# Kernel tuning notes

Measured on AMD Instinct MI355X. Metric: run time of the kernel, lower is better.

Reference implementation:

```python
import jax, jax.numpy as jnp
import numpy as np

# Dimensions
N = 20000      # nodes
E = 320000     # edges (avg degree 16)
B = 4          # batchsize (independent weight replicas)
F_IN = 128     # nfeat
H = 128        # nhid[0]
C = 64         # nclass


def setup_inputs() -> dict:
    key = jax.random.key(0)
    ks = jax.random.split(key, 9)
    x = jax.random.normal(ks[0], (N, F_IN), dtype=jnp.float32)
    adj_rows = jax.random.randint(ks[1], (E,), 0, N, dtype=jnp.int32)
    adj_cols = jax.random.randint(ks[2], (E,), 0, N, dtype=jnp.int32)
    # positive normalized-ish edge weights (like a normalized adjacency)
    adj_vals = jax.random.uniform(ks[3], (E,), dtype=jnp.float32) / 16.0
    # GraphConvolution weights: uniform(-stdv, stdv), stdv = 1/sqrt(out_features)
    s0 = 1.0 / np.sqrt(H)
    s1 = 1.0 / np.sqrt(C)
    w0 = jax.random.uniform(ks[4], (B, F_IN, H), dtype=jnp.float32, minval=-s0, maxval=s0)
    w1 = jax.random.uniform(ks[5], (B, H, C), dtype=jnp.float32, minval=-s1, maxval=s1)
    # per-batch Linear(nclass, 1) heads, stacked
    sr = 1.0 / np.sqrt(C)
    reg_w = jax.random.uniform(ks[6], (B, C), dtype=jnp.float32, minval=-sr, maxval=sr)
    reg_b = jax.random.uniform(ks[7], (B,), dtype=jnp.float32, minval=-sr, maxval=sr)
    return dict(x=x, adj_rows=adj_rows, adj_cols=adj_cols, adj_vals=adj_vals,
                w0=w0, w1=w1, reg_w=reg_w, reg_b=reg_b)


def _gcn_layer(h, w, rows, cols, vals):
    # h: [N, B, in], w: [B, in, out]
    support = jnp.einsum('nbi,bio->nbo', h, w)          # per-batch dense GEMM
    s_flat = support.reshape(N, -1)                     # [N, B*out]
    # spmm: out[r] += val * s_flat[c] for each edge (r, c)
    msgs = vals[:, None] * s_flat[cols]                 # [E, B*out]
    out = jax.ops.segment_sum(msgs, rows, num_segments=N)
    return out.reshape(N, B, -1)                        # [N, B, out]


def reference(x, adj_rows, adj_cols, adj_vals, w0, w1, reg_w, reg_b):
    # eval mode: dropout is identity
    h = jnp.broadcast_to(x[:, None, :], (N, B, F_IN))   # expand + transpose(0,1)
    h = jax.nn.relu(_gcn_layer(h, w0, adj_rows, adj_cols, adj_vals))
    h = _gcn_layer(h, w1, adj_rows, adj_cols, adj_vals)  # [N, B, C]
    hT = h.transpose(1, 0, 2)                            # [B, N, C]
    y = jnp.einsum('bnc,bc->bn', hT, reg_w) + reg_b[:, None]
    return y
```

## Files before the change

### kernel.cpp

```cpp
#include <hip/hip_runtime.h>
#include <hip/hip_bf16.h>


#define NN 20000
#define EE 320000
#define BB 4
#define FF 128
#define HH 128
#define CC 64
#define DEGW 64

typedef unsigned short u16;
typedef short short8 __attribute__((ext_vector_type(8)));
typedef float floatx4 __attribute__((ext_vector_type(4)));

static __device__ __forceinline__ float b2f(u16 u) {
    union { unsigned int i; float f; } x;
    x.i = ((unsigned int)u) << 16;
    return x.f;
}

static __device__ __forceinline__ u16 f2b(float f) {
    __hip_bfloat16 h = __float2bfloat16(f);
    return *reinterpret_cast<u16*>(&h);
}


__global__ void k_pre(int* __restrict__ deg,
                      const float* __restrict__ x, u16* __restrict__ xb,
                      const float* __restrict__ w0, const float* __restrict__ w1,
                      const float* __restrict__ regw, u16* __restrict__ w0t,
                      float* __restrict__ v1) {
    int gid = blockIdx.x * 256 + threadIdx.x;
    if (gid < NN) deg[gid] = 0;
    if (gid < NN * FF / 4) {
        float4 v = ((const float4*)x)[gid];
        ushort4 o;
        o.x = f2b(v.x); o.y = f2b(v.y); o.z = f2b(v.z); o.w = f2b(v.w);
        ((ushort4*)xb)[gid] = o;
    }
    if (gid < BB * FF * HH) {
        int b = gid >> 14;
        int rem = gid & 16383;
        int h = rem >> 7;
        int k = rem & 127;
        w0t[gid] = f2b(w0[(b << 14) + (k << 7) + h]);
    }
    if (gid < BB * HH) {
        int b = gid >> 7;
        int h = gid & 127;
        const float* wrow = w1 + (b * HH + h) * CC;
        const float* rw = regw + b * CC;
        float s = 0.f;
#pragma unroll
        for (int c = 0; c < CC; ++c) s += wrow[c] * rw[c];
        v1[gid] = s;
    }
}


__global__ void k_scatter(const int* __restrict__ rows, const int* __restrict__ cols,
                          const float* __restrict__ vals, int* __restrict__ deg,
                          uint2* __restrict__ epack) {
    int e = blockIdx.x * 256 + threadIdx.x;
    if (e < EE) {
        int r = rows[e];
        int p = atomicAdd(&deg[r], 1);
        epack[(r << 6) + p] = make_uint2((unsigned)cols[e], __float_as_uint(vals[e]));
    }
}


__global__ void k_spmm(const int* __restrict__ deg, const uint2* __restrict__ epack,
                       const u16* __restrict__ xb, u16* __restrict__ xa) {
    int wave = (blockIdx.x * 256 + threadIdx.x) >> 6;
    int lane = threadIdx.x & 63;
    if (wave >= NN) return;
    int d = deg[wave];
    int eg = lane >> 3;
    int fl = lane & 7;
    int p0 = wave << 6;
    float acc[16];
#pragma unroll
    for (int j = 0; j < 16; ++j) acc[j] = 0.f;
    for (int p = eg; p < d; p += 8) {
        uint2 ep = epack[p0 + p];
        float v = __uint_as_float(ep.y);
        const u16* xr = xb + (((size_t)ep.x) << 7) + fl * 16;
        short8 x0 = *(const short8*)(xr);
        short8 x1 = *(const short8*)(xr + 8);
#pragma unroll
        for (int j = 0; j < 8; ++j) {
            acc[j]     += v * b2f((u16)x0[j]);
            acc[8 + j] += v * b2f((u16)x1[j]);
        }
    }
#pragma unroll
    for (int j = 0; j < 16; ++j) {
        acc[j] += __shfl_xor(acc[j], 8);
        acc[j] += __shfl_xor(acc[j], 16);
        acc[j] += __shfl_xor(acc[j], 32);
    }
    if (eg == 0) {
        short8 o0, o1;
#pragma unroll
        for (int j = 0; j < 8; ++j) {
            o0[j] = (short)f2b(acc[j]);
            o1[j] = (short)f2b(acc[8 + j]);
        }
        u16* orow = xa + (((size_t)wave) << 7) + fl * 16;
        *(short8*)(orow) = o0;
        *(short8*)(orow + 8) = o1;
    }
}


__global__ __launch_bounds__(256) void k_gemm(const u16* __restrict__ xa,
                                              const u16* __restrict__ w0t,
                                              const float* __restrict__ v1,
                                              float* __restrict__ z) {
    __shared__ u16 sA[128 * 64];
    __shared__ u16 sB[128 * 64];
    __shared__ float part[2][128];

    int b = blockIdx.y;
    int rowbase = blockIdx.x * 128;
    int t = threadIdx.x;
    int wid = t >> 6;
    int lane = t & 63;
    int wr = wid >> 1;
    int wc = wid & 1;
    int g = lane >> 4;
    int lr = lane & 15;

    floatx4 acc[4][4];
#pragma unroll
    for (int i = 0; i < 4; ++i)
#pragma unroll
        for (int j = 0; j < 4; ++j) acc[i][j] = (floatx4){0.f, 0.f, 0.f, 0.f};

#pragma unroll
    for (int ks = 0; ks < 2; ++ks) {
#pragma unroll
        for (int it = 0; it < 4; ++it) {
            int idx = it * 256 + t;
            int r = idx >> 3;
            int c = idx & 7;
            int sl = c ^ (r & 7);
            uint4 av = make_uint4(0u, 0u, 0u, 0u);
            int grow = rowbase + r;
            if (grow < NN) av = *(const uint4*)(xa + (((size_t)grow) << 7) + ks * 64 + c * 8);
            *(uint4*)(&sA[r * 64 + sl * 8]) = av;
            uint4 bv = *(const uint4*)(w0t + (((size_t)b) << 14) + (r << 7) + ks * 64 + c * 8);
            *(uint4*)(&sB[r * 64 + sl * 8]) = bv;
        }
        __syncthreads();

#pragma unroll
        for (int kk = 0; kk < 2; ++kk) {
            short8 a[4], bv[4];
#pragma unroll
            for (int i = 0; i < 4; ++i) {
                int row = wr * 64 + i * 16 + lr;
                int slot = (kk * 4 + g) ^ (row & 7);
                a[i] = *(const short8*)(&sA[row * 64 + slot * 8]);
            }
#pragma unroll
            for (int j = 0; j < 4; ++j) {
                int h = wc * 64 + j * 16 + lr;
                int slot = (kk * 4 + g) ^ (h & 7);
                bv[j] = *(const short8*)(&sB[h * 64 + slot * 8]);
            }
#pragma unroll
            for (int i = 0; i < 4; ++i)
#pragma unroll
                for (int j = 0; j < 4; ++j)
                    acc[i][j] = __builtin_amdgcn_mfma_f32_16x16x32_bf16(a[i], bv[j], acc[i][j], 0, 0, 0);
        }
        __syncthreads();
    }

    float vv[4];
#pragma unroll
    for (int j = 0; j < 4; ++j) vv[j] = v1[b * 128 + wc * 64 + j * 16 + lr];

#pragma unroll
    for (int i = 0; i < 4; ++i) {
#pragma unroll
        for (int r = 0; r < 4; ++r) {
            float s = 0.f;
#pragma unroll
            for (int j = 0; j < 4; ++j) s += fmaxf(acc[i][j][r], 0.f) * vv[j];
            s += __shfl_xor(s, 1);
            s += __shfl_xor(s, 2);
            s += __shfl_xor(s, 4);
            s += __shfl_xor(s, 8);
            if (lr == 0) part[wc][wr * 64 + i * 16 + g * 4 + r] = s;
        }
    }
    __syncthreads();
    if (t < 128) {
        int grow = rowbase + t;
        if (grow < NN) z[grow * 4 + b] = part[0][t] + part[1][t];
    }
}


__global__ void k_spmv(const int* __restrict__ deg, const uint2* __restrict__ epack,
                       const float* __restrict__ z, const float* __restrict__ regb,
                       float* __restrict__ y) {
    int wave = (blockIdx.x * 256 + threadIdx.x) >> 6;
    int lane = threadIdx.x & 63;
    if (wave >= NN) return;
    int d = deg[wave];
    int eg = lane >> 2;
    int b = lane & 3;
    int p0 = wave << 6;
    float acc = 0.f;
    for (int p = eg; p < d; p += 16) {
        uint2 ep = epack[p0 + p];
        acc += __uint_as_float(ep.y) * z[(((size_t)ep.x) << 2) + b];
    }
    acc += __shfl_xor(acc, 4);
    acc += __shfl_xor(acc, 8);
    acc += __shfl_xor(acc, 16);
    acc += __shfl_xor(acc, 32);
    if (lane < 4) y[lane * NN + wave] = acc + regb[lane];
}


extern "C" void kernel_launch(void* const* d_in, const int* in_sizes, int n_in,
                              void* d_out, int out_size, void* d_ws, size_t ws_size,
                              hipStream_t stream) {
    const float* x    = (const float*)d_in[0];
    const int*   rows = (const int*)d_in[1];
    const int*   cols = (const int*)d_in[2];
    const float* vals = (const float*)d_in[3];
    const float* w0   = (const float*)d_in[4];
    const float* w1   = (const float*)d_in[5];
    const float* regw = (const float*)d_in[6];
    const float* regb = (const float*)d_in[7];
    float* y = (float*)d_out;

    char* ws = (char*)d_ws;
    int*   deg   = (int*)(ws + 0);
    uint2* epack = (uint2*)(ws + 81920);
    u16*   xb    = (u16*)(ws + 10321920);
    u16*   xa    = (u16*)(ws + 15441920);
    u16*   w0t   = (u16*)(ws + 20561920);
    float* v1    = (float*)(ws + 20692992);
    float* z     = (float*)(ws + 20695040);

    k_pre<<<(NN * FF / 4 + 255) / 256, 256, 0, stream>>>(deg, x, xb, w0, w1, regw, w0t, v1);
    k_scatter<<<(EE + 255) / 256, 256, 0, stream>>>(rows, cols, vals, deg, epack);
    k_spmm<<<(NN * 64) / 256, 256, 0, stream>>>(deg, epack, xb, xa);
    dim3 ggemm((NN + 127) / 128, BB);
    k_gemm<<<ggemm, 256, 0, stream>>>(xa, w0t, v1, z);
    k_spmv<<<(NN * 64 + 255) / 256, 256, 0, stream>>>(deg, epack, z, regb, y);
}
```

Baseline: 127.4 us.

## Fuse SpMM with per-batch GEMM and merge scatter into preprocessing kernel

The SpMM is fused with the first-layer GEMM. Each 512-thread block aggregates 64 rows into swizzled shared memory, then runs the MFMA GEMM for all four batch replicas on those rows, so the intermediate xa never travels through global memory. The edge scatter moves into the init kernel, and the degree counters are zeroed with a memset instead, which removes one kernel launch. In exchange, the B operand is now read directly from global memory rather than staged in LDS, and the fused block runs the latency-bound gather and the MFMA phases one after the other with no overlap.

Result: slower. 155.0 us (+21.6%).

```diff
diff --git a/kernel.cpp b/kernel.cpp
--- a/kernel.cpp
+++ b/kernel.cpp
@@ -8,7 +8,6 @@
 #define FF 128
 #define HH 128
 #define CC 64
-#define DEGW 64
 
 typedef unsigned short u16;
 typedef short short8 __attribute__((ext_vector_type(8)));
@@ -26,13 +25,19 @@
 }
 
 
-__global__ void k_pre(int* __restrict__ deg,
-                      const float* __restrict__ x, u16* __restrict__ xb,
-                      const float* __restrict__ w0, const float* __restrict__ w1,
-                      const float* __restrict__ regw, u16* __restrict__ w0t,
-                      float* __restrict__ v1) {
+__global__ void k_init(const int* __restrict__ rows, const int* __restrict__ cols,
+                       const float* __restrict__ vals, int* __restrict__ deg,
+                       uint2* __restrict__ epack,
+                       const float* __restrict__ x, u16* __restrict__ xb,
+                       const float* __restrict__ w0, const float* __restrict__ w1,
+                       const float* __restrict__ regw, u16* __restrict__ w0t,
+                       float* __restrict__ v1) {
     int gid = blockIdx.x * 256 + threadIdx.x;
-    if (gid < NN) deg[gid] = 0;
+    if (gid < EE) {
+        int r = rows[gid];
+        int p = atomicAdd(&deg[r], 1);
+        epack[(r << 6) + p] = make_uint2((unsigned)cols[gid], __float_as_uint(vals[gid]));
+    }
     if (gid < NN * FF / 4) {
         float4 v = ((const float4*)x)[gid];
         ushort4 o;
@@ -59,149 +64,124 @@
 }
 
 
-__global__ void k_scatter(const int* __restrict__ rows, const int* __restrict__ cols,
-                          const float* __restrict__ vals, int* __restrict__ deg,
-                          uint2* __restrict__ epack) {
-    int e = blockIdx.x * 256 + threadIdx.x;
-    if (e < EE) {
-        int r = rows[e];
-        int p = atomicAdd(&deg[r], 1);
-        epack[(r << 6) + p] = make_uint2((unsigned)cols[e], __float_as_uint(vals[e]));
-    }
-}
-
-
-__global__ void k_spmm(const int* __restrict__ deg, const uint2* __restrict__ epack,
-                       const u16* __restrict__ xb, u16* __restrict__ xa) {
-    int wave = (blockIdx.x * 256 + threadIdx.x) >> 6;
-    int lane = threadIdx.x & 63;
-    if (wave >= NN) return;
-    int d = deg[wave];
-    int eg = lane >> 3;
-    int fl = lane & 7;
-    int p0 = wave << 6;
-    float acc[16];
-#pragma unroll
-    for (int j = 0; j < 16; ++j) acc[j] = 0.f;
-    for (int p = eg; p < d; p += 8) {
-        uint2 ep = epack[p0 + p];
-        float v = __uint_as_float(ep.y);
-        const u16* xr = xb + (((size_t)ep.x) << 7) + fl * 16;
-        short8 x0 = *(const short8*)(xr);
-        short8 x1 = *(const short8*)(xr + 8);
-#pragma unroll
-        for (int j = 0; j < 8; ++j) {
-            acc[j]     += v * b2f((u16)x0[j]);
-            acc[8 + j] += v * b2f((u16)x1[j]);
+__global__ __launch_bounds__(512) void k_spmm_gemm(const int* __restrict__ deg,
+                                                   const uint2* __restrict__ epack,
+                                                   const u16* __restrict__ xb,
+                                                   const u16* __restrict__ w0t,
+                                                   const float* __restrict__ v1,
+                                                   float* __restrict__ z) {
+    __shared__ u16 sA[64 * 128];
+    __shared__ float part[BB][2][64];
+
+    int base = blockIdx.x * 64;
+    int t = threadIdx.x;
+    int wv = t >> 6;
+    int lane = t & 63;
+
+    {
+        int eg = lane >> 3;
+        int fl = lane & 7;
+#pragma unroll
+        for (int it = 0; it < 8; ++it) {
+            int lr0 = wv * 8 + it;
+            int row = base + lr0;
+            int d = (row < NN) ? deg[row] : 0;
+            float acc[16];
+#pragma unroll
+            for (int j = 0; j < 16; ++j) acc[j] = 0.f;
+            int p0 = row << 6;
+            for (int p = eg; p < d; p += 8) {
+                uint2 ep = epack[p0 + p];
+                float v = __uint_as_float(ep.y);
+                const u16* xr = xb + (((size_t)ep.x) << 7) + fl * 16;
+                short8 x0 = *(const short8*)(xr);
+                short8 x1 = *(const short8*)(xr + 8);
+#pragma unroll
+                for (int j = 0; j < 8; ++j) {
+                    acc[j]     += v * b2f((u16)x0[j]);
+                    acc[8 + j] += v * b2f((u16)x1[j]);
+                }
+            }
+#pragma unroll
+            for (int j = 0; j < 16; ++j) {
+                acc[j] += __shfl_xor(acc[j], 8);
+                acc[j] += __shfl_xor(acc[j], 16);
+                acc[j] += __shfl_xor(acc[j], 32);
+            }
+            if (eg == 0) {
+                short8 o0, o1;
+#pragma unroll
+                for (int j = 0; j < 8; ++j) {
+                    o0[j] = (short)f2b(acc[j]);
+                    o1[j] = (short)f2b(acc[8 + j]);
+                }
+                int c0 = 2 * fl, c1 = 2 * fl + 1;
+                *(short8*)(&sA[lr0 * 128 + (c0 ^ (lr0 & 7)) * 8]) = o0;
+                *(short8*)(&sA[lr0 * 128 + (c1 ^ (lr0 & 7)) * 8]) = o1;
+            }
         }
     }
-#pragma unroll
-    for (int j = 0; j < 16; ++j) {
-        acc[j] += __shfl_xor(acc[j], 8);
-        acc[j] += __shfl_xor(acc[j], 16);
-        acc[j] += __shfl_xor(acc[j], 32);
-    }
-    if (eg == 0) {
-        short8 o0, o1;
-#pragma unroll
-        for (int j = 0; j < 8; ++j) {
-            o0[j] = (short)f2b(acc[j]);
-            o1[j] = (short)f2b(acc[8 + j]);
-        }
-        u16* orow = xa + (((size_t)wave) << 7) + fl * 16;
-        *(short8*)(orow) = o0;
-        *(short8*)(orow + 8) = o1;
-    }
-}
-
-
-__global__ __launch_bounds__(256) void k_gemm(const u16* __restrict__ xa,
-                                              const u16* __restrict__ w0t,
-                                              const float* __restrict__ v1,
-                                              float* __restrict__ z) {
-    __shared__ u16 sA[128 * 64];
-    __shared__ u16 sB[128 * 64];
-    __shared__ float part[2][128];
-
-    int b = blockIdx.y;
-    int rowbase = blockIdx.x * 128;
-    int t = threadIdx.x;
-    int wid = t >> 6;
-    int lane = t & 63;
-    int wr = wid >> 1;
-    int wc = wid & 1;
-    int g = lane >> 4;
-    int lr = lane & 15;
-
-    floatx4 acc[4][4];
-#pragma unroll
-    for (int i = 0; i < 4; ++i)
-#pragma unroll
-        for (int j = 0; j < 4; ++j) acc[i][j] = (floatx4){0.f, 0.f, 0.f, 0.f};
-
-#pragma unroll
-    for (int ks = 0; ks < 2; ++ks) {
-#pragma unroll
-        for (int it = 0; it < 4; ++it) {
-            int idx = it * 256 + t;
-            int r = idx >> 3;
-            int c = idx & 7;
-            int sl = c ^ (r & 7);
-            uint4 av = make_uint4(0u, 0u, 0u, 0u);
-            int grow = rowbase + r;
-            if (grow < NN) av = *(const uint4*)(xa + (((size_t)grow) << 7) + ks * 64 + c * 8);
-            *(uint4*)(&sA[r * 64 + sl * 8]) = av;
-            uint4 bv = *(const uint4*)(w0t + (((size_t)b) << 14) + (r << 7) + ks * 64 + c * 8);
-            *(uint4*)(&sB[r * 64 + sl * 8]) = bv;
-        }
-        __syncthreads();
-
-#pragma unroll
-        for (int kk = 0; kk < 2; ++kk) {
-            short8 a[4], bv[4];
+    __syncthreads();
+
+    {
+        int b = wv >> 1;
+        int wc = wv & 1;
+        int g = lane >> 4;
+        int lr = lane & 15;
+
+        floatx4 acc[4][4];
+#pragma unroll
+        for (int i = 0; i < 4; ++i)
+#pragma unroll
+            for (int j = 0; j < 4; ++j) acc[i][j] = (floatx4){0.f, 0.f, 0.f, 0.f};
+
+#pragma unroll
+        for (int kk = 0; kk < 4; ++kk) {
+            short8 a[4], bf[4];
 #pragma unroll
             for (int i = 0; i < 4; ++i) {
-                int row = wr * 64 + i * 16 + lr;
+                int row = i * 16 + lr;
                 int slot = (kk * 4 + g) ^ (row & 7);
-                a[i] = *(const short8*)(&sA[row * 64 + slot * 8]);
+                a[i] = *(const short8*)(&sA[row * 128 + slot * 8]);
             }
 #pragma unroll
             for (int j = 0; j < 4; ++j) {
                 int h = wc * 64 + j * 16 + lr;
-                int slot = (kk * 4 + g) ^ (h & 7);
-                bv[j] = *(const short8*)(&sB[h * 64 + slot * 8]);
+                bf[j] = *(const short8*)(w0t + (((size_t)b) << 14) + (h << 7) + kk * 32 + g * 8);
             }
 #pragma unroll
             for (int i = 0; i < 4; ++i)
 #pragma unroll
                 for (int j = 0; j < 4; ++j)
-                    acc[i][j] = __builtin_amdgcn_mfma_f32_16x16x32_bf16(a[i], bv[j], acc[i][j], 0, 0, 0);
+                    acc[i][j] = __builtin_amdgcn_mfma_f32_16x16x32_bf16(a[i], bf[j], acc[i][j], 0, 0, 0);
         }
-        __syncthreads();
-    }
-
-    float vv[4];
-#pragma unroll
-    for (int j = 0; j < 4; ++j) vv[j] = v1[b * 128 + wc * 64 + j * 16 + lr];
-
-#pragma unroll
-    for (int i = 0; i < 4; ++i) {
-#pragma unroll
-        for (int r = 0; r < 4; ++r) {
-            float s = 0.f;
-#pragma unroll
-            for (int j = 0; j < 4; ++j) s += fmaxf(acc[i][j][r], 0.f) * vv[j];
-            s += __shfl_xor(s, 1);
-            s += __shfl_xor(s, 2);
-            s += __shfl_xor(s, 4);
-            s += __shfl_xor(s, 8);
-            if (lr == 0) part[wc][wr * 64 + i * 16 + g * 4 + r] = s;
+
+        float vv[4];
+#pragma unroll
+        for (int j = 0; j < 4; ++j) vv[j] = v1[b * 128 + wc * 64 + j * 16 + lr];
+
+#pragma unroll
+        for (int i = 0; i < 4; ++i) {
+#pragma unroll
+            for (int r = 0; r < 4; ++r) {
+                float s = 0.f;
+#pragma unroll
+                for (int j = 0; j < 4; ++j) s += fmaxf(acc[i][j][r], 0.f) * vv[j];
+                s += __shfl_xor(s, 1);
+                s += __shfl_xor(s, 2);
+                s += __shfl_xor(s, 4);
+                s += __shfl_xor(s, 8);
+                if (lr == 0) part[b][wc][i * 16 + g * 4 + r] = s;
+            }
         }
     }
     __syncthreads();
-    if (t < 128) {
-        int grow = rowbase + t;
-        if (grow < NN) z[grow * 4 + b] = part[0][t] + part[1][t];
+
+    if (t < 256) {
+        int b = t >> 6;
+        int r = t & 63;
+        int grow = base + r;
+        if (grow < NN) z[grow * 4 + b] = part[b][0][r] + part[b][1][r];
     }
 }
 
@@ -246,15 +226,13 @@
     int*   deg   = (int*)(ws + 0);
     uint2* epack = (uint2*)(ws + 81920);
     u16*   xb    = (u16*)(ws + 10321920);
-    u16*   xa    = (u16*)(ws + 15441920);
-    u16*   w0t   = (u16*)(ws + 20561920);
-    float* v1    = (float*)(ws + 20692992);
-    float* z     = (float*)(ws + 20695040);
-
-    k_pre<<<(NN * FF / 4 + 255) / 256, 256, 0, stream>>>(deg, x, xb, w0, w1, regw, w0t, v1);
-    k_scatter<<<(EE + 255) / 256, 256, 0, stream>>>(rows, cols, vals, deg, epack);
-    k_spmm<<<(NN * 64) / 256, 256, 0, stream>>>(deg, epack, xb, xa);
-    dim3 ggemm((NN + 127) / 128, BB);
-    k_gemm<<<ggemm, 256, 0, stream>>>(xa, w0t, v1, z);
+    u16*   w0t   = (u16*)(ws + 15441920);
+    float* v1    = (float*)(ws + 15572992);
+    float* z     = (float*)(ws + 15575040);
+
+    hipMemsetAsync(deg, 0, NN * sizeof(int), stream);
+    k_init<<<(NN * FF / 4 + 255) / 256, 256, 0, stream>>>(rows, cols, vals, deg, epack,
+                                                          x, xb, w0, w1, regw, w0t, v1);
+    k_spmm_gemm<<<(NN + 63) / 64, 512, 0, stream>>>(deg, epack, xb, w0t, v1, z);
     k_spmv<<<(NN * 64 + 255) / 256, 256, 0, stream>>>(deg, epack, z, regb, y);
 }
```
